# Optimization experiments

Hardware: AMD Instinct MI355X
Metric: run time of the kernel (lower is better)

Reference implementation:

```python
import jax, jax.numpy as jnp
import numpy as np

V_SIZE = 128000  # vocab size (v_size init arg)


def setup_inputs() -> dict:
    key = jax.random.key(0)
    k1, k2 = jax.random.split(key)
    # per-position scores -> weighting_scheme (softmax over seq dim)
    w_es = jax.random.normal(k1, (256, 2048), dtype=jnp.float32)
    # instance['x']: token ids in [0, v_size)
    x = jax.random.randint(k2, (256, 2048), 0, V_SIZE, dtype=jnp.int64)
    return {"w_es": w_es, "x": x}


def reference(w_es, x):
    # weighting_scheme(indices, w_es, instance): softmax over sequence positions
    weights = jax.nn.softmax(w_es, axis=-1)          # [B, S]
    B, S = weights.shape
    rows = jnp.arange(B)[:, None]                    # [B, 1] broadcast against [B, S]
    # scatter: w_a[b, x[b, i]] = weights[b, i]  (vectorized index_put)
    w_a = jnp.zeros((B, V_SIZE), dtype=weights.dtype).at[rows, x].set(weights)
    return (w_a, weights)
```

## Files before the change

kernel.cpp:

```cpp
#include <hip/hip_runtime.h>

#define BATCH 256
#define SEQ   2048
#define VOCAB 128000
#define CHUNK 16384
#define CPR   8

typedef float v4f __attribute__((ext_vector_type(4)));
typedef int   v4i __attribute__((ext_vector_type(4)));
typedef float v2f __attribute__((ext_vector_type(2)));
typedef int   v2i __attribute__((ext_vector_type(2)));

__global__ __launch_bounds__(1024, 4)
void softmax_scatter_chunked(const float* __restrict__ w_es,
                             const int*   __restrict__ x,
                             float* __restrict__ w_a,
                             float* __restrict__ w_out)
{
    __shared__ int   chunk[CHUNK];
    __shared__ float red[32];

    const int bid = blockIdx.x;
    const int r = bid & (BATCH - 1);
    const int c = bid >> 8;
    const int base = c * CHUNK;
    const int cnt  = (VOCAB - base < CHUNK) ? (VOCAB - base) : CHUNK;
    const int cnt4 = cnt >> 2;

    const int t = threadIdx.x;
    const int lane = t & 63;
    const int wid  = t >> 6;

    {
        const v4i m1 = (v4i)(-1);
        #pragma unroll
        for (int j = 0; j < (CHUNK >> 2); j += 1024)
            ((v4i*)chunk)[j + t] = m1;
    }

    const float* rowp = w_es + (size_t)r * SEQ;
    const v2f a = ((const v2f*)rowp)[t];

    float m = fmaxf(a.x, a.y);
    #pragma unroll
    for (int off = 32; off > 0; off >>= 1)
        m = fmaxf(m, __shfl_down(m, off, 64));
    if (lane == 0) red[wid] = m;
    __syncthreads();
    m = red[0];
    #pragma unroll
    for (int k = 1; k < 16; ++k) m = fmaxf(m, red[k]);

    const float e0 = __expf(a.x - m);
    const float e1 = __expf(a.y - m);
    float s = e0 + e1;
    #pragma unroll
    for (int off = 32; off > 0; off >>= 1)
        s += __shfl_down(s, off, 64);
    if (lane == 0) red[16 + wid] = s;
    __syncthreads();
    s = red[16];
    #pragma unroll
    for (int k = 1; k < 16; ++k) s += red[16 + k];

    const float inv = 1.0f / s;
    const float w0 = e0 * inv;
    const float w1 = e1 * inv;

    if (c == 0) {
        v2f wv; wv.x = w0; wv.y = w1;
        ((v2f*)(w_out + (size_t)r * SEQ))[t] = wv;
    }

    const v2i xv = ((const v2i*)(x + (size_t)r * SEQ))[t];
    const int i0 = 2 * t;
    const int i1 = 2 * t + 1;
    const int v0 = xv.x - base;
    const int v1 = xv.y - base;
    const bool in0 = (unsigned)v0 < (unsigned)cnt;
    const bool in1 = (unsigned)v1 < (unsigned)cnt;

    if (in0) atomicMax(&chunk[v0], i0);
    if (in1) atomicMax(&chunk[v1], i1);
    __syncthreads();

    if (in0 && chunk[v0] == i0) ((float*)chunk)[v0] = w0;
    if (in1 && chunk[v1] == i1) ((float*)chunk)[v1] = w1;
    __syncthreads();

    float* gp = w_a + (size_t)r * VOCAB + base;
    #pragma unroll 4
    for (int j = t; j < cnt4; j += 1024) {
        v4i b = ((const v4i*)chunk)[j];
        v4f o;
        o.x = (b.x < 0) ? 0.0f : __int_as_float(b.x);
        o.y = (b.y < 0) ? 0.0f : __int_as_float(b.y);
        o.z = (b.z < 0) ? 0.0f : __int_as_float(b.z);
        o.w = (b.w < 0) ? 0.0f : __int_as_float(b.w);
        ((v4f*)(gp))[j] = o;
    }
}

extern "C" void kernel_launch(void* const* d_in, const int* in_sizes, int n_in,
                              void* d_out, int out_size, void* d_ws, size_t ws_size,
                              hipStream_t stream) {
    const float* w_es = (const float*)d_in[0];
    const int*   x    = (const int*)d_in[1];

    float* out  = (float*)d_out;
    float* w_a  = out;
    float* w    = out + (size_t)BATCH * VOCAB;

    softmax_scatter_chunked<<<BATCH * CPR, 1024, 0, stream>>>(w_es, x, w_a, w);
}
```

Measured before the change: 135.9 us.

## Process each row half in four LDS phases to amortize softmax recompute

Instead of 8 blocks per row each recomputing the row softmax and reloading indices, the kernel launches 2 blocks per row. Each block loops over four 16000-entry vocab phases, reusing the softmax weights and index registers, and reinitializes LDS between phases. Barriers are replaced by a lightweight LDS-only waitcnt plus s_barrier. This cuts redundant softmax and index-load work but lowers grid parallelism to 512 blocks and adds serialized phases with extra barriers.

```diff
diff --git a/kernel.cpp b/kernel.cpp
--- a/kernel.cpp
+++ b/kernel.cpp
@@ -3,29 +3,31 @@
 #define BATCH 256
 #define SEQ   2048
 #define VOCAB 128000
-#define CHUNK 16384
-#define CPR   8
+#define HALF   64000
+#define PCHUNK 16000
+#define NPH    4
 
 typedef float v4f __attribute__((ext_vector_type(4)));
 typedef int   v4i __attribute__((ext_vector_type(4)));
 typedef float v2f __attribute__((ext_vector_type(2)));
 typedef int   v2i __attribute__((ext_vector_type(2)));
 
+#define LBAR() do { asm volatile("s_waitcnt lgkmcnt(0)" ::: "memory"); \
+                    __builtin_amdgcn_s_barrier(); } while (0)
+
 __global__ __launch_bounds__(1024, 4)
-void softmax_scatter_chunked(const float* __restrict__ w_es,
-                             const int*   __restrict__ x,
-                             float* __restrict__ w_a,
-                             float* __restrict__ w_out)
+void softmax_scatter_phased(const float* __restrict__ w_es,
+                            const int*   __restrict__ x,
+                            float* __restrict__ w_a,
+                            float* __restrict__ w_out)
 {
-    __shared__ int   chunk[CHUNK];
+    __shared__ int   chunk[PCHUNK];
     __shared__ float red[32];
 
     const int bid = blockIdx.x;
     const int r = bid & (BATCH - 1);
-    const int c = bid >> 8;
-    const int base = c * CHUNK;
-    const int cnt  = (VOCAB - base < CHUNK) ? (VOCAB - base) : CHUNK;
-    const int cnt4 = cnt >> 2;
+    const int h = bid >> 8;
+    const int base0 = h * HALF;
 
     const int t = threadIdx.x;
     const int lane = t & 63;
@@ -34,8 +36,10 @@
     {
         const v4i m1 = (v4i)(-1);
         #pragma unroll
-        for (int j = 0; j < (CHUNK >> 2); j += 1024)
-            ((v4i*)chunk)[j + t] = m1;
+        for (int j0 = 0; j0 < 4096; j0 += 1024) {
+            const int j = j0 + t;
+            if (j < (PCHUNK >> 2)) ((v4i*)chunk)[j] = m1;
+        }
     }
 
     const float* rowp = w_es + (size_t)r * SEQ;
@@ -67,7 +71,7 @@
     const float w0 = e0 * inv;
     const float w1 = e1 * inv;
 
-    if (c == 0) {
+    if (h == 0) {
         v2f wv; wv.x = w0; wv.y = w1;
         ((v2f*)(w_out + (size_t)r * SEQ))[t] = wv;
     }
@@ -75,29 +79,49 @@
     const v2i xv = ((const v2i*)(x + (size_t)r * SEQ))[t];
     const int i0 = 2 * t;
     const int i1 = 2 * t + 1;
-    const int v0 = xv.x - base;
-    const int v1 = xv.y - base;
-    const bool in0 = (unsigned)v0 < (unsigned)cnt;
-    const bool in1 = (unsigned)v1 < (unsigned)cnt;
 
-    if (in0) atomicMax(&chunk[v0], i0);
-    if (in1) atomicMax(&chunk[v1], i1);
-    __syncthreads();
+    float* const growp = w_a + (size_t)r * VOCAB;
 
-    if (in0 && chunk[v0] == i0) ((float*)chunk)[v0] = w0;
-    if (in1 && chunk[v1] == i1) ((float*)chunk)[v1] = w1;
-    __syncthreads();
+    for (int p = 0; p < NPH; ++p) {
+        const int pb = base0 + p * PCHUNK;
+        const int v0 = xv.x - pb;
+        const int v1 = xv.y - pb;
+        const bool in0 = (unsigned)v0 < (unsigned)PCHUNK;
+        const bool in1 = (unsigned)v1 < (unsigned)PCHUNK;
 
-    float* gp = w_a + (size_t)r * VOCAB + base;
-    #pragma unroll 4
-    for (int j = t; j < cnt4; j += 1024) {
-        v4i b = ((const v4i*)chunk)[j];
-        v4f o;
-        o.x = (b.x < 0) ? 0.0f : __int_as_float(b.x);
-        o.y = (b.y < 0) ? 0.0f : __int_as_float(b.y);
-        o.z = (b.z < 0) ? 0.0f : __int_as_float(b.z);
-        o.w = (b.w < 0) ? 0.0f : __int_as_float(b.w);
-        ((v4f*)(gp))[j] = o;
+        if (in0) atomicMax(&chunk[v0], i0);
+        if (in1) atomicMax(&chunk[v1], i1);
+        LBAR();
+
+        if (in0 && chunk[v0] == i0) ((float*)chunk)[v0] = w0;
+        if (in1 && chunk[v1] == i1) ((float*)chunk)[v1] = w1;
+        LBAR();
+
+        float* gp = growp + pb;
+        #pragma unroll
+        for (int j0 = 0; j0 < 4096; j0 += 1024) {
+            const int j = j0 + t;
+            if (j < (PCHUNK >> 2)) {
+                v4i b = ((const v4i*)chunk)[j];
+                v4f o;
+                o.x = (b.x < 0) ? 0.0f : __int_as_float(b.x);
+                o.y = (b.y < 0) ? 0.0f : __int_as_float(b.y);
+                o.z = (b.z < 0) ? 0.0f : __int_as_float(b.z);
+                o.w = (b.w < 0) ? 0.0f : __int_as_float(b.w);
+                ((v4f*)gp)[j] = o;
+            }
+        }
+
+        if (p < NPH - 1) {
+            LBAR();
+            const v4i m1 = (v4i)(-1);
+            #pragma unroll
+            for (int j0 = 0; j0 < 4096; j0 += 1024) {
+                const int j = j0 + t;
+                if (j < (PCHUNK >> 2)) ((v4i*)chunk)[j] = m1;
+            }
+            LBAR();
+        }
     }
 }
 
@@ -111,5 +135,5 @@
     float* w_a  = out;
     float* w    = out + (size_t)BATCH * VOCAB;
 
-    softmax_scatter_chunked<<<BATCH * CPR, 1024, 0, stream>>>(w_es, x, w_a, w);
+    softmax_scatter_phased<<<2 * BATCH, 1024, 0, stream>>>(w_es, x, w_a, w);
 }
```

After: 136.6 us. Within noise of the previous version (+0.6%).
